# Kernel tuning notes

Measured on AMD Instinct MI355X. Metric: run time of the kernel, lower is better.

Reference implementation:

```python
import jax, jax.numpy as jnp
import numpy as np

# Probabilistic Conway forward prop: for each cell, let p_i be the live
# probability of its 8 Moore neighbors (torus wrap via roll). The output is
# P(exactly 3 live neighbors) + P(exactly 2 live neighbors) * p_self.
# The original enumerates all C(8,2)=28 and C(8,3)=56 combinations of
# degree-8 products; here we compute the identical Poisson-binomial pmf
# values with the standard DP recurrence pmf_k <- pmf_k*(1-p) + pmf_{k-1}*p,
# truncated at k=3 (truncation does not affect pmf_2 / pmf_3).

MOORE_OFFSETS = [(i, j) for i in (-1, 0, 1) for j in (-1, 0, 1) if (i, j) != (0, 0)]


def setup_inputs() -> dict:
    key = jax.random.key(0)
    inputs = jax.random.uniform(key, (32, 1024, 1024), dtype=jnp.float32)
    return {"inputs": inputs}


def reference(inputs):
    pmf0 = jnp.ones_like(inputs)
    pmf1 = jnp.zeros_like(inputs)
    pmf2 = jnp.zeros_like(inputs)
    pmf3 = jnp.zeros_like(inputs)
    for shift in MOORE_OFFSETS:  # fixed 8-iteration stencil loop
        p = jnp.roll(inputs, shift, axis=(-2, -1))
        q = 1.0 - p
        pmf3 = pmf3 * q + pmf2 * p
        pmf2 = pmf2 * q + pmf1 * p
        pmf1 = pmf1 * q + pmf0 * p
        pmf0 = pmf0 * q
    # P(live next) = P(3 live nbrs) + P(2 live nbrs) * P(self live)
    return pmf3 + pmf2 * inputs
```

## Files before the change

kernel.cpp:

```cpp
#include <hip/hip_runtime.h>


#define H 1024
#define W 1024
#define RPT 4
#define NROWS (RPT + 2)

typedef float f32x4 __attribute__((ext_vector_type(4)));
typedef float f32x2 __attribute__((ext_vector_type(2)));

__global__ __launch_bounds__(256) void prob_conway_kernel(
    const float* __restrict__ in, float* __restrict__ out) {
    const int nblk = 32 * (H / RPT);
    const int cpx  = nblk / 8;
    const int bid  = blockIdx.x;
    const int s    = (bid & 7) * cpx + (bid >> 3);

    const int plane = s >> 8;
    const int rg    = s & 255;
    const int r0    = rg * RPT;
    const int lane  = threadIdx.x & 63;
    const int c0    = threadIdx.x * 4;

    const float* __restrict__ img = in + (size_t)plane * (H * W);
    float* __restrict__ o         = out + (size_t)plane * (H * W);

    const int wbase = (threadIdx.x >> 6) << 8;
    const int clw   = (wbase + W - 1) & (W - 1);
    const int crw   = (wbase + 256) & (W - 1);
    int gi = lane >> 1;
    gi = (gi < NROWS) ? gi : 0;
    const int grow = (r0 + gi - 1 + H) & (H - 1);
    const int gcol = (lane & 1) ? crw : clw;
    const float gv = img[(size_t)grow * W + gcol];

    float P[NROWS][6];
    if (rg != 0 && rg != 255) {
        const float* rp = img + (size_t)(r0 - 1) * W + c0;
#pragma unroll
        for (int i = 0; i < NROWS; ++i) {
            const f32x4 v = *reinterpret_cast<const f32x4*>(rp);
            P[i][1] = v.x; P[i][2] = v.y; P[i][3] = v.z; P[i][4] = v.w;
            rp += W;
        }
    } else {
#pragma unroll
        for (int i = 0; i < NROWS; ++i) {
            const int r = (r0 + i - 1 + H) & (H - 1);
            const f32x4 v =
                *reinterpret_cast<const f32x4*>(img + (size_t)r * W + c0);
            P[i][1] = v.x; P[i][2] = v.y; P[i][3] = v.z; P[i][4] = v.w;
        }
    }

#pragma unroll
    for (int i = 0; i < NROWS; ++i) {
        const float lv = __shfl_up(P[i][4], 1);
        const float rv = __shfl_down(P[i][1], 1);
        const float e  = __shfl(gv, 2 * i + ((lane == 63) ? 1 : 0));
        P[i][0] = (lane == 0)  ? e : lv;
        P[i][5] = (lane == 63) ? e : rv;
    }

    f32x2 Q[4][6];
#pragma unroll
    for (int i = 0; i < 4; ++i)
#pragma unroll
        for (int c = 0; c < 6; ++c)
            Q[i][c] = f32x2{P[i][c], P[i + 2][c]};

#pragma unroll
    for (int k = 0; k < 2; ++k) {
        f32x2 v3[6][4];
        f32x2 dd[4][3];
#pragma unroll
        for (int jc = 0; jc < 6; ++jc) {
            const f32x2 a  = Q[k][jc];
            const f32x2 b  = Q[k + 1][jc];
            const f32x2 cc = Q[k + 2][jc];
            const f32x2 qa = 1.0f - a, qb = 1.0f - b, qc = 1.0f - cc;
            const f32x2 d0 = qa * qc;
            const f32x2 d1 = qa * cc + a * qc;
            const f32x2 d2 = a * cc;
            v3[jc][0] = d0 * qb;
            v3[jc][1] = d1 * qb + d0 * b;
            v3[jc][2] = d2 * qb + d1 * b;
            v3[jc][3] = d2 * b;
            if (jc >= 1 && jc <= 4) {
                dd[jc - 1][0] = d0; dd[jc - 1][1] = d1; dd[jc - 1][2] = d2;
            }
        }
        f32x2 res[4];
#pragma unroll
        for (int x = 0; x < 4; ++x) {
            const f32x2* L = v3[x];
            const f32x2* R = v3[x + 2];
            const f32x2* D = dd[x];
            const f32x2 w0 = L[0] * R[0];
            const f32x2 w1 = L[1] * R[0] + L[0] * R[1];
            const f32x2 w2 = L[2] * R[0] + L[1] * R[1] + L[0] * R[2];
            const f32x2 w3 = L[3] * R[0] + L[2] * R[1] + L[1] * R[2] + L[0] * R[3];
            const f32x2 pmf2 = w2 * D[0] + w1 * D[1] + w0 * D[2];
            const f32x2 pmf3 = w3 * D[0] + w2 * D[1] + w1 * D[2];
            res[x] = pmf3 + pmf2 * Q[k + 1][x + 1];
        }
        const f32x4 lo = {res[0].x, res[1].x, res[2].x, res[3].x};
        const f32x4 hi = {res[0].y, res[1].y, res[2].y, res[3].y};
        __builtin_nontemporal_store(
            lo, reinterpret_cast<f32x4*>(o + (size_t)(r0 + k) * W + c0));
        __builtin_nontemporal_store(
            hi, reinterpret_cast<f32x4*>(o + (size_t)(r0 + k + 2) * W + c0));
    }
}

extern "C" void kernel_launch(void* const* d_in, const int* in_sizes, int n_in,
                              void* d_out, int out_size, void* d_ws, size_t ws_size,
                              hipStream_t stream) {
    const float* in = (const float*)d_in[0];
    float* out = (float*)d_out;
    dim3 grid(32 * (H / RPT));
    dim3 block(256);
    prob_conway_kernel<<<grid, block, 0, stream>>>(in, out);
}
```

Before: 43.96 us.

## Process four planes per block with double-buffered register prefetch

```diff
diff --git a/kernel.cpp b/kernel.cpp
--- a/kernel.cpp
+++ b/kernel.cpp
@@ -4,26 +4,91 @@
 #define H 1024
 #define W 1024
 #define RPT 4
-#define NROWS (RPT + 2)
+#define NROWS 6
+#define ITERS 4
 
 typedef float f32x4 __attribute__((ext_vector_type(4)));
 typedef float f32x2 __attribute__((ext_vector_type(2)));
 
+struct Consume {
+    int lane, c0, r0;
+    float* o;
+
+    __device__ __forceinline__ void run(const f32x4 (&buf)[NROWS], float gv) {
+        float P[NROWS][6];
+#pragma unroll
+        for (int i = 0; i < NROWS; ++i) {
+            P[i][1] = buf[i].x; P[i][2] = buf[i].y;
+            P[i][3] = buf[i].z; P[i][4] = buf[i].w;
+        }
+#pragma unroll
+        for (int i = 0; i < NROWS; ++i) {
+            const float lv = __shfl_up(P[i][4], 1);
+            const float rv = __shfl_down(P[i][1], 1);
+            const float e  = __shfl(gv, 2 * i + ((lane == 63) ? 1 : 0));
+            P[i][0] = (lane == 0)  ? e : lv;
+            P[i][5] = (lane == 63) ? e : rv;
+        }
+        f32x2 Q[4][6];
+#pragma unroll
+        for (int i = 0; i < 4; ++i)
+#pragma unroll
+            for (int c = 0; c < 6; ++c)
+                Q[i][c] = f32x2{P[i][c], P[i + 2][c]};
+#pragma unroll
+        for (int k = 0; k < 2; ++k) {
+            f32x2 v3[6][4];
+            f32x2 dd[4][3];
+#pragma unroll
+            for (int jc = 0; jc < 6; ++jc) {
+                const f32x2 a  = Q[k][jc];
+                const f32x2 b  = Q[k + 1][jc];
+                const f32x2 cc = Q[k + 2][jc];
+                const f32x2 qa = 1.0f - a, qb = 1.0f - b, qc = 1.0f - cc;
+                const f32x2 d0 = qa * qc;
+                const f32x2 d1 = qa * cc + a * qc;
+                const f32x2 d2 = a * cc;
+                v3[jc][0] = d0 * qb;
+                v3[jc][1] = d1 * qb + d0 * b;
+                v3[jc][2] = d2 * qb + d1 * b;
+                v3[jc][3] = d2 * b;
+                if (jc >= 1 && jc <= 4) {
+                    dd[jc - 1][0] = d0; dd[jc - 1][1] = d1; dd[jc - 1][2] = d2;
+                }
+            }
+            f32x2 res[4];
+#pragma unroll
+            for (int x = 0; x < 4; ++x) {
+                const f32x2* L = v3[x];
+                const f32x2* R = v3[x + 2];
+                const f32x2* D = dd[x];
+                const f32x2 w0 = L[0] * R[0];
+                const f32x2 w1 = L[1] * R[0] + L[0] * R[1];
+                const f32x2 w2 = L[2] * R[0] + L[1] * R[1] + L[0] * R[2];
+                const f32x2 w3 = L[3] * R[0] + L[2] * R[1] + L[1] * R[2]
+                               + L[0] * R[3];
+                const f32x2 pmf2 = w2 * D[0] + w1 * D[1] + w0 * D[2];
+                const f32x2 pmf3 = w3 * D[0] + w2 * D[1] + w1 * D[2];
+                res[x] = pmf3 + pmf2 * Q[k + 1][x + 1];
+            }
+            const f32x4 lo = {res[0].x, res[1].x, res[2].x, res[3].x};
+            const f32x4 hi = {res[0].y, res[1].y, res[2].y, res[3].y};
+            __builtin_nontemporal_store(
+                lo, reinterpret_cast<f32x4*>(o + (size_t)(r0 + k) * W + c0));
+            __builtin_nontemporal_store(
+                hi, reinterpret_cast<f32x4*>(o + (size_t)(r0 + k + 2) * W + c0));
+        }
+    }
+};
+
 __global__ __launch_bounds__(256) void prob_conway_kernel(
     const float* __restrict__ in, float* __restrict__ out) {
-    const int nblk = 32 * (H / RPT);
-    const int cpx  = nblk / 8;
     const int bid  = blockIdx.x;
-    const int s    = (bid & 7) * cpx + (bid >> 3);
-
-    const int plane = s >> 8;
-    const int rg    = s & 255;
-    const int r0    = rg * RPT;
-    const int lane  = threadIdx.x & 63;
-    const int c0    = threadIdx.x * 4;
-
-    const float* __restrict__ img = in + (size_t)plane * (H * W);
-    float* __restrict__ o         = out + (size_t)plane * (H * W);
+    const int xcd  = bid & 7;
+    const int rg   = bid >> 3;
+    const int r0   = rg * RPT;
+    const int lane = threadIdx.x & 63;
+    const int c0   = threadIdx.x * 4;
 
     const int wbase = (threadIdx.x >> 6) << 8;
     const int clw   = (wbase + W - 1) & (W - 1);
@@ -32,85 +97,41 @@
     gi = (gi < NROWS) ? gi : 0;
     const int grow = (r0 + gi - 1 + H) & (H - 1);
     const int gcol = (lane & 1) ? crw : clw;
-    const float gv = img[(size_t)grow * W + gcol];
+    const size_t goff = (size_t)grow * W + gcol;
 
-    float P[NROWS][6];
-    if (rg != 0 && rg != 255) {
-        const float* rp = img + (size_t)(r0 - 1) * W + c0;
+    size_t rowoff[NROWS];
 #pragma unroll
-        for (int i = 0; i < NROWS; ++i) {
-            const f32x4 v = *reinterpret_cast<const f32x4*>(rp);
-            P[i][1] = v.x; P[i][2] = v.y; P[i][3] = v.z; P[i][4] = v.w;
-            rp += W;
-        }
-    } else {
-#pragma unroll
-        for (int i = 0; i < NROWS; ++i) {
-            const int r = (r0 + i - 1 + H) & (H - 1);
-            const f32x4 v =
-                *reinterpret_cast<const f32x4*>(img + (size_t)r * W + c0);
-            P[i][1] = v.x; P[i][2] = v.y; P[i][3] = v.z; P[i][4] = v.w;
-        }
+    for (int i = 0; i < NROWS; ++i)
+        rowoff[i] = (size_t)((r0 + i - 1 + H) & (H - 1)) * W + c0;
+
+    f32x4 bufA[NROWS], bufB[NROWS];
+    float gvA, gvB;
+
+#define ISSUE(buf, gvv, it_next)                                          \
+    {                                                                     \
+        const float* img = in + (size_t)((it_next) * 8 + xcd) * (H * W);  \
+        _Pragma("unroll")                                                 \
+        for (int i = 0; i < NROWS; ++i)                                   \
+            buf[i] = *reinterpret_cast<const f32x4*>(img + rowoff[i]);    \
+        gvv = img[goff];                                                  \
     }
 
-#pragma unroll
-    for (int i = 0; i < NROWS; ++i) {
-        const float lv = __shfl_up(P[i][4], 1);
-        const float rv = __shfl_down(P[i][1], 1);
-        const float e  = __shfl(gv, 2 * i + ((lane == 63) ? 1 : 0));
-        P[i][0] = (lane == 0)  ? e : lv;
-        P[i][5] = (lane == 63) ? e : rv;
-    }
+    ISSUE(bufA, gvA, 0)
 
-    f32x2 Q[4][6];
-#pragma unroll
-    for (int i = 0; i < 4; ++i)
-#pragma unroll
-        for (int c = 0; c < 6; ++c)
-            Q[i][c] = f32x2{P[i][c], P[i + 2][c]};
+    Consume cns;
+    cns.lane = lane; cns.c0 = c0; cns.r0 = r0;
 
 #pragma unroll
-    for (int k = 0; k < 2; ++k) {
-        f32x2 v3[6][4];
-        f32x2 dd[4][3];
-#pragma unroll
-        for (int jc = 0; jc < 6; ++jc) {
-            const f32x2 a  = Q[k][jc];
-            const f32x2 b  = Q[k + 1][jc];
-            const f32x2 cc = Q[k + 2][jc];
-            const f32x2 qa = 1.0f - a, qb = 1.0f - b, qc = 1.0f - cc;
-            const f32x2 d0 = qa * qc;
-            const f32x2 d1 = qa * cc + a * qc;
-            const f32x2 d2 = a * cc;
-            v3[jc][0] = d0 * qb;
-            v3[jc][1] = d1 * qb + d0 * b;
-            v3[jc][2] = d2 * qb + d1 * b;
-            v3[jc][3] = d2 * b;
-            if (jc >= 1 && jc <= 4) {
-                dd[jc - 1][0] = d0; dd[jc - 1][1] = d1; dd[jc - 1][2] = d2;
-            }
+    for (int it = 0; it < ITERS; ++it) {
+        if (it + 1 < ITERS) {
+            if ((it & 1) == 0) ISSUE(bufB, gvB, it + 1)
+            else               ISSUE(bufA, gvA, it + 1)
         }
-        f32x2 res[4];
-#pragma unroll
-        for (int x = 0; x < 4; ++x) {
-            const f32x2* L = v3[x];
-            const f32x2* R = v3[x + 2];
-            const f32x2* D = dd[x];
-            const f32x2 w0 = L[0] * R[0];
-            const f32x2 w1 = L[1] * R[0] + L[0] * R[1];
-            const f32x2 w2 = L[2] * R[0] + L[1] * R[1] + L[0] * R[2];
-            const f32x2 w3 = L[3] * R[0] + L[2] * R[1] + L[1] * R[2] + L[0] * R[3];
-            const f32x2 pmf2 = w2 * D[0] + w1 * D[1] + w0 * D[2];
-            const f32x2 pmf3 = w3 * D[0] + w2 * D[1] + w1 * D[2];
-            res[x] = pmf3 + pmf2 * Q[k + 1][x + 1];
-        }
-        const f32x4 lo = {res[0].x, res[1].x, res[2].x, res[3].x};
-        const f32x4 hi = {res[0].y, res[1].y, res[2].y, res[3].y};
-        __builtin_nontemporal_store(
-            lo, reinterpret_cast<f32x4*>(o + (size_t)(r0 + k) * W + c0));
-        __builtin_nontemporal_store(
-            hi, reinterpret_cast<f32x4*>(o + (size_t)(r0 + k + 2) * W + c0));
+        cns.o = out + (size_t)(it * 8 + xcd) * (H * W);
+        if ((it & 1) == 0) cns.run(bufA, gvA);
+        else               cns.run(bufB, gvB);
     }
+#undef ISSUE
 }
 
 extern "C" void kernel_launch(void* const* d_in, const int* in_sizes, int n_in,
@@ -118,7 +139,7 @@
                               hipStream_t stream) {
     const float* in = (const float*)d_in[0];
     float* out = (float*)d_out;
-    dim3 grid(32 * (H / RPT));
+    dim3 grid(2048);
     dim3 block(256);
     prob_conway_kernel<<<grid, block, 0, stream>>>(in, out);
 }
```

Result: slower. 44.96 us (+2.3%).
